# Kernel tuning notes

Hardware: AMD Instinct MI355X
Metric: run time of the kernel (lower is better)

Reference implementation:

```python
import jax, jax.numpy as jnp
import numpy as np

TOP_K = 4  # config.ffn_config.moe_top_k


def setup_inputs() -> dict:
    key = jax.random.key(0)
    k1, k2, k3, k4 = jax.random.split(key, 4)
    T, D, I, E = 4096, 1024, 2048, 16
    hidden_states = jax.random.normal(k1, (T, D), dtype=jnp.float32)
    router_w = jax.random.normal(k2, (E, D), dtype=jnp.float32) * 0.02
    # ws stacks [w1; v1] along output dim: [E, 2*I, D]
    ws = jax.random.normal(k3, (E, 2 * I, D), dtype=jnp.float32) * 0.02
    # w2s: [E, D, I]
    w2s = jax.random.normal(k4, (E, D, I), dtype=jnp.float32) * 0.02
    return {"hidden_states": hidden_states, "router_w": router_w, "ws": ws, "w2s": w2s}


def reference(hidden_states, router_w, ws, w2s):
    T, D = hidden_states.shape
    E = router_w.shape[0]
    I = ws.shape[1] // 2

    # Router: ReplicatedLinear(d_model -> num_experts), no bias
    router_logits = hidden_states @ router_w.T                      # [T, E]

    # fused_moe gating: softmax over all experts, top-k, renormalize
    probs = jax.nn.softmax(router_logits, axis=-1)                  # [T, E]
    topk_vals, topk_idx = jax.lax.top_k(probs, TOP_K)               # [T, K]
    topk_vals = topk_vals / jnp.sum(topk_vals, axis=-1, keepdims=True)
    # dense gate matrix [T, E]: selected experts get renormalized weight, else 0
    gates = jnp.zeros((T, E), dtype=hidden_states.dtype)
    gates = gates.at[jnp.arange(T)[:, None], topk_idx].set(topk_vals)

    h = jnp.einsum('td,eid->tei', hidden_states, ws)                # [T, E, 2I]
    act = jax.nn.silu(h[..., :I]) * h[..., I:]                      # [T, E, I]
    y = jnp.einsum('tei,edi->ted', act, w2s)                        # [T, E, D]

    # Combine: weighted sum over selected experts
    return jnp.einsum('ted,te->td', y, gates)                       # [T, D]
```

## Files before the change

kernel.cpp:

```cpp
#include <hip/hip_runtime.h>
#include <hip/hip_bf16.h>

#define T_TOK 4096
#define D_MODEL 1024
#define I_DIM 2048
#define E_EXP 16

typedef __bf16 bf16x8 __attribute__((ext_vector_type(8)));
typedef float f32x4 __attribute__((ext_vector_type(4)));

__device__ __forceinline__ bf16x8 pack8(f32x4 a, f32x4 b) {
    bf16x8 r;
    r[0] = (__bf16)a[0]; r[1] = (__bf16)a[1]; r[2] = (__bf16)a[2]; r[3] = (__bf16)a[3];
    r[4] = (__bf16)b[0]; r[5] = (__bf16)b[1]; r[6] = (__bf16)b[2]; r[7] = (__bf16)b[3];
    return r;
}

__device__ __forceinline__ void gl2lds(const __bf16* src, __bf16* dst) {
    __builtin_amdgcn_global_load_lds(
        (const __attribute__((address_space(1))) unsigned int*)src,
        (__attribute__((address_space(3))) unsigned int*)dst, 16, 0, 0);
}

__global__ __launch_bounds__(256) void cvt_kernel(
    const float* __restrict__ in, __bf16* __restrict__ out, int n8)
{
    const int stride = gridDim.x * 256;
    for (int i = blockIdx.x * 256 + threadIdx.x; i < n8; i += stride) {
        f32x4 a = ((const f32x4*)in)[i * 2];
        f32x4 b = ((const f32x4*)in)[i * 2 + 1];
        ((bf16x8*)out)[i] = pack8(a, b);
    }
}

__global__ __launch_bounds__(256) void router_fused_kernel(
    const float* __restrict__ x, const float* __restrict__ rw,
    unsigned int* __restrict__ choices, float* __restrict__ gate4,
    __bf16* __restrict__ x_bf, const float* __restrict__ wsw, __bf16* __restrict__ ws_bf)
{
    const int b = blockIdx.x;
    if (b >= 1280) {
        const int n8 = E_EXP * 2 * I_DIM * D_MODEL / 8;
        for (int i = (b - 1280) * 256 + threadIdx.x; i < n8; i += 2048 * 256) {
            f32x4 a = ((const f32x4*)wsw)[i * 2];
            f32x4 c = ((const f32x4*)wsw)[i * 2 + 1];
            ((bf16x8*)ws_bf)[i] = pack8(a, c);
        }
        return;
    }
    if (b >= 1024) {
        const int n8 = T_TOK * D_MODEL / 8;
        for (int i = (b - 1024) * 256 + threadIdx.x; i < n8; i += 256 * 256) {
            f32x4 a = ((const f32x4*)x)[i * 2];
            f32x4 c = ((const f32x4*)x)[i * 2 + 1];
            ((bf16x8*)x_bf)[i] = pack8(a, c);
        }
        return;
    }
    const int wid = threadIdx.x >> 6, lane = threadIdx.x & 63;
    const int t = b * 4 + wid;
    const int e = lane & 15, part = lane >> 4;

    const float* xr = x + (size_t)t * D_MODEL + part * 256;
    const float* wr = rw + (size_t)e * D_MODEL + part * 256;
    double acc = 0.0;
    #pragma unroll 4
    for (int i = 0; i < 256; i += 4) {
        f32x4 xv = *(const f32x4*)(xr + i);
        f32x4 wv = *(const f32x4*)(wr + i);
        acc += (double)xv[0] * wv[0] + (double)xv[1] * wv[1]
             + (double)xv[2] * wv[2] + (double)xv[3] * wv[3];
    }
    acc += __shfl_xor(acc, 16, 64);
    acc += __shfl_xor(acc, 32, 64);

    __shared__ float logits[4][16];
    if (lane < 16) logits[wid][lane] = (float)acc;
    __syncthreads();

    if (lane == 0) {
        float l[16];
        #pragma unroll
        for (int i = 0; i < 16; i++) l[i] = logits[wid][i];
        int idx[4]; float val[4];
        unsigned taken = 0;
        for (int k = 0; k < 4; k++) {
            int best = 0; float bv = -1e30f;
            for (int i = 0; i < 16; i++)
                if (!((taken >> i) & 1) && l[i] > bv) { bv = l[i]; best = i; }
            idx[k] = best; val[k] = bv; taken |= (1u << best);
        }
        const float m = val[0];
        float w[4], s = 0.f;
        for (int k = 0; k < 4; k++) { w[k] = __expf(val[k] - m); s += w[k]; }
        choices[t] = (unsigned)idx[0] | ((unsigned)idx[1] << 4)
                   | ((unsigned)idx[2] << 8) | ((unsigned)idx[3] << 12);
        f32x4 g = {w[0] / s, w[1] / s, w[2] / s, w[3] / s};
        *(f32x4*)(gate4 + t * 4) = g;
    }
}

__global__ __launch_bounds__(256) void build_lists_kernel(
    const unsigned int* __restrict__ choices, const float* __restrict__ gate4,
    int* __restrict__ counts, int* __restrict__ tok_list, float* __restrict__ gate_list)
{
    const int e = blockIdx.x;
    const int tid = threadIdx.x, lane = tid & 63, w = tid >> 6;
    __shared__ int wave_cnt[4];
    __shared__ int running;
    if (tid == 0) running = 0;
    __syncthreads();
    for (int chunk = 0; chunk < T_TOK; chunk += 256) {
        const int t = chunk + tid;
        const unsigned int ch = choices[t];
        int k = -1;
        #pragma unroll
        for (int kk = 0; kk < 4; ++kk)
            if (((ch >> (4 * kk)) & 15u) == (unsigned)e) k = kk;
        const unsigned long long m = __ballot(k >= 0);
        const int my = __popcll(m & ((1ull << lane) - 1ull));
        if (lane == 0) wave_cnt[w] = __popcll(m);
        __syncthreads();
        int base = running;
        #pragma unroll
        for (int i = 0; i < 4; ++i) if (i < w) base += wave_cnt[i];
        if (k >= 0) {
            const int slot = base + my;
            tok_list[e * T_TOK + slot] = t;
            gate_list[e * T_TOK + slot] = gate4[t * 4 + k];
        }
        __syncthreads();
        if (tid == 0) running += wave_cnt[0] + wave_cnt[1] + wave_cnt[2] + wave_cnt[3];
        __syncthreads();
    }
    if (tid == 0) counts[e] = running;
}

__global__ void prefix_kernel(const int* __restrict__ counts, int* __restrict__ prefix) {
    if (threadIdx.x == 0) {
        int acc = 0;
        for (int e = 0; e < E_EXP; e++) { prefix[e] = acc; acc += (counts[e] + 255) & ~255; }
        prefix[E_EXP] = acc;
    }
}

__global__ __launch_bounds__(256, 3) void gemm1_kernel(
    const __bf16* __restrict__ xb, const __bf16* __restrict__ wsb,
    const int* __restrict__ counts, const int* __restrict__ prefix,
    const int* __restrict__ tok_list, __bf16* __restrict__ act)
{
    const int q8 = gridDim.x >> 3;
    const int lid = (blockIdx.x & 7) * q8 + (blockIdx.x >> 3);
    const int e = lid >> 9;
    const int r = lid & 511;
    const int tileM = r & 15;
    const int tileN = r >> 4;

    const int count = counts[e];
    if (tileM * 128 >= count) return;

    const int tid = threadIdx.x;
    const int lane = tid & 63, w = tid >> 6;
    const int l15 = lane & 15, q = lane >> 4, l7 = lane & 7;
    const int wm = w >> 1, wc = w & 1;

    __shared__ __bf16 As[128 * 64];
    __shared__ __bf16 Bs[128 * 64];

    const int rl = lane >> 3;
    const int lc = (lane & 7) ^ rl;
    const __bf16* ptrA[4]; const __bf16* ptrB[4];
    #pragma unroll
    for (int i = 0; i < 4; ++i) {
        int grow = tileM * 128 + w * 32 + i * 8 + rl;
        if (grow >= count) grow = count - 1;
        const int token = tok_list[e * T_TOK + grow];
        ptrA[i] = xb + (size_t)token * D_MODEL + lc * 8;
        const int sub = w * 32 + i * 8 + rl;
        const int gcol = (sub < 64) ? (tileN * 64 + sub) : (I_DIM + tileN * 64 + (sub - 64));
        ptrB[i] = wsb + ((size_t)e * 2 * I_DIM + gcol) * D_MODEL + lc * 8;
    }
    __bf16* dA = &As[w * 2048];
    __bf16* dB = &Bs[w * 2048];

    #define STAGE(koff) do { \
        _Pragma("unroll") \
        for (int i_ = 0; i_ < 4; ++i_) gl2lds(ptrA[i_] + (koff), dA + i_ * 512); \
        _Pragma("unroll") \
        for (int i_ = 0; i_ < 4; ++i_) gl2lds(ptrB[i_] + (koff), dB + i_ * 512); \
    } while (0)

    f32x4 acc[4][4];
    const f32x4 z = {0.f, 0.f, 0.f, 0.f};
    #pragma unroll
    for (int mi = 0; mi < 4; ++mi)
        #pragma unroll
        for (int nj = 0; nj < 4; ++nj) acc[mi][nj] = z;

    const int c0 = (q ^ l7) * 8, c1 = ((4 + q) ^ l7) * 8;
    const int aoff = (wm * 64 + l15) * 64;
    const int boff = (wc * 32 + l15) * 64;

    STAGE(0);
    for (int kt = 0; kt < 16; ++kt) {
        __syncthreads();
        bf16x8 a0[4], a1[4], b0[4], b1[4];
        #pragma unroll
        for (int mi = 0; mi < 4; ++mi) {
            a0[mi] = *(const bf16x8*)&As[aoff + mi * 1024 + c0];
            a1[mi] = *(const bf16x8*)&As[aoff + mi * 1024 + c1];
        }
        #pragma unroll
        for (int nj = 0; nj < 2; ++nj) {
            b0[nj]     = *(const bf16x8*)&Bs[boff + nj * 1024 + c0];
            b0[nj + 2] = *(const bf16x8*)&Bs[boff + 4096 + nj * 1024 + c0];
            b1[nj]     = *(const bf16x8*)&Bs[boff + nj * 1024 + c1];
            b1[nj + 2] = *(const bf16x8*)&Bs[boff + 4096 + nj * 1024 + c1];
        }
        __syncthreads();
        if (kt + 1 < 16) STAGE((kt + 1) * 64);
        #pragma unroll
        for (int mi = 0; mi < 4; ++mi)
            #pragma unroll
            for (int nj = 0; nj < 4; ++nj) {
                acc[mi][nj] = __builtin_amdgcn_mfma_f32_16x16x32_bf16(a0[mi], b0[nj], acc[mi][nj], 0, 0, 0);
                acc[mi][nj] = __builtin_amdgcn_mfma_f32_16x16x32_bf16(a1[mi], b1[nj], acc[mi][nj], 0, 0, 0);
            }
    }
    #undef STAGE

    const int abase = prefix[e];
    #pragma unroll
    for (int mi = 0; mi < 4; ++mi) {
        #pragma unroll
        for (int j = 0; j < 4; ++j) {
            const int grow = tileM * 128 + wm * 64 + mi * 16 + q * 4 + j;
            if (grow < count) {
                __bf16* arowp = act + (size_t)(abase + grow) * I_DIM + tileN * 64 + wc * 32 + l15;
                #pragma unroll
                for (int nj = 0; nj < 2; ++nj) {
                    const float v1 = acc[mi][nj][j];
                    const float v2 = acc[mi][nj + 2][j];
                    arowp[nj * 16] = (__bf16)(v1 / (1.f + __expf(-v1)) * v2);
                }
            }
        }
    }
}

__global__ __launch_bounds__(256, 3) void gemm2_kernel(
    const __bf16* __restrict__ act, const __bf16* __restrict__ w2b,
    const int* __restrict__ counts, const int* __restrict__ prefix,
    const int* __restrict__ tok_list, const float* __restrict__ gate_list,
    float* __restrict__ out)
{
    const int q8 = gridDim.x >> 3;
    const int lid = (blockIdx.x & 7) * q8 + (blockIdx.x >> 3);
    const int e = lid >> 8;
    const int r = lid & 255;
    const int tileM = r & 15;
    const int tileN = (r >> 4) & 7;
    const int h = r >> 7;

    const int count = counts[e];
    if (tileM * 128 >= count) return;

    const int tid = threadIdx.x;
    const int lane = tid & 63, w = tid >> 6;
    const int l15 = lane & 15, q = lane >> 4, l7 = lane & 7;
    const int wm = w >> 1, wc = w & 1;
    const int abase = prefix[e];

    __shared__ __bf16 As[128 * 64];
    __shared__ __bf16 Bs[128 * 64];

    const int rl = lane >> 3;
    const int lc = (lane & 7) ^ rl;
    const __bf16* ptrA[4]; const __bf16* ptrB[4];
    #pragma unroll
    for (int i = 0; i < 4; ++i) {
        const int ar = tileM * 128 + w * 32 + i * 8 + rl;
        ptrA[i] = act + (size_t)(abase + ar) * I_DIM + h * 1024 + lc * 8;
        const int dcol = tileN * 128 + w * 32 + i * 8 + rl;
        ptrB[i] = w2b + ((size_t)e * D_MODEL + dcol) * I_DIM + h * 1024 + lc * 8;
    }
    __bf16* dA = &As[w * 2048];
    __bf16* dB = &Bs[w * 2048];

    #define STAGE(koff) do { \
        _Pragma("unroll") \
        for (int i_ = 0; i_ < 4; ++i_) gl2lds(ptrA[i_] + (koff), dA + i_ * 512); \
        _Pragma("unroll") \
        for (int i_ = 0; i_ < 4; ++i_) gl2lds(ptrB[i_] + (koff), dB + i_ * 512); \
    } while (0)

    f32x4 acc[4][4];
    const f32x4 z = {0.f, 0.f, 0.f, 0.f};
    #pragma unroll
    for (int mi = 0; mi < 4; ++mi)
        #pragma unroll
        for (int nj = 0; nj < 4; ++nj) acc[mi][nj] = z;

    const int c0 = (q ^ l7) * 8, c1 = ((4 + q) ^ l7) * 8;
    const int aoff = (wm * 64 + l15) * 64;
    const int boff = (wc * 64 + l15) * 64;

    STAGE(0);
    for (int kt = 0; kt < 16; ++kt) {
        __syncthreads();
        bf16x8 a0[4], a1[4], b0[4], b1[4];
        #pragma unroll
        for (int mi = 0; mi < 4; ++mi) {
            a0[mi] = *(const bf16x8*)&As[aoff + mi * 1024 + c0];
            a1[mi] = *(const bf16x8*)&As[aoff + mi * 1024 + c1];
        }
        #pragma unroll
        for (int nj = 0; nj < 4; ++nj) {
            b0[nj] = *(const bf16x8*)&Bs[boff + nj * 1024 + c0];
            b1[nj] = *(const bf16x8*)&Bs[boff + nj * 1024 + c1];
        }
        __syncthreads();
        if (kt + 1 < 16) STAGE((kt + 1) * 64);
        #pragma unroll
        for (int mi = 0; mi < 4; ++mi)
            #pragma unroll
            for (int nj = 0; nj < 4; ++nj) {
                acc[mi][nj] = __builtin_amdgcn_mfma_f32_16x16x32_bf16(a0[mi], b0[nj], acc[mi][nj], 0, 0, 0);
                acc[mi][nj] = __builtin_amdgcn_mfma_f32_16x16x32_bf16(a1[mi], b1[nj], acc[mi][nj], 0, 0, 0);
            }
    }
    #undef STAGE

    #pragma unroll
    for (int mi = 0; mi < 4; ++mi) {
        #pragma unroll
        for (int j = 0; j < 4; ++j) {
            const int grow = tileM * 128 + wm * 64 + mi * 16 + q * 4 + j;
            if (grow < count) {
                const int token = tok_list[e * T_TOK + grow];
                const float gate = gate_list[e * T_TOK + grow];
                float* orow = out + (size_t)token * D_MODEL + tileN * 128 + wc * 64 + l15;
                #pragma unroll
                for (int nj = 0; nj < 4; ++nj)
                    atomicAdd(orow + nj * 16, gate * acc[mi][nj][j]);
            }
        }
    }
}

extern "C" void kernel_launch(void* const* d_in, const int* in_sizes, int n_in,
                              void* d_out, int out_size, void* d_ws, size_t ws_size,
                              hipStream_t stream)
{
    const float* x   = (const float*)d_in[0];
    const float* rw  = (const float*)d_in[1];
    const float* wsw = (const float*)d_in[2];
    const float* w2s = (const float*)d_in[3];
    float* out = (float*)d_out;

    char* wsb = (char*)d_ws;
    int* counts        = (int*)wsb;
    int* prefix        = (int*)(wsb + 128);
    int* tok_list      = (int*)(wsb + 1024);
    float* gate_list   = (float*)(wsb + 1024 + E_EXP * T_TOK * 4);
    unsigned* choices  = (unsigned*)(wsb + 544u * 1024);
    float* gate4       = (float*)(wsb + 576u * 1024);
    __bf16* x_bf       = (__bf16*)(wsb + (1u << 20));
    __bf16* act        = (__bf16*)(wsb + (12u << 20));
    __bf16* ws_bf      = (__bf16*)(wsb + (96u << 20));
    __bf16* w2_bf      = ws_bf;

    hipMemsetAsync(d_out, 0, (size_t)out_size * sizeof(float), stream);

    router_fused_kernel<<<dim3(3328), 256, 0, stream>>>(x, rw, choices, gate4, x_bf, wsw, ws_bf);
    build_lists_kernel<<<dim3(E_EXP), 256, 0, stream>>>(choices, gate4, counts, tok_list, gate_list);
    prefix_kernel<<<1, 64, 0, stream>>>(counts, prefix);

    gemm1_kernel<<<dim3(8192), 256, 0, stream>>>(
        x_bf, ws_bf, counts, prefix, tok_list, act);

    cvt_kernel<<<8192, 256, 0, stream>>>(w2s, w2_bf, E_EXP * D_MODEL * I_DIM / 8);

    gemm2_kernel<<<dim3(4096), 256, 0, stream>>>(
        act, w2_bf, counts, prefix, tok_list, gate_list, out);
}
```

Before: 502.8 us.

## Replace atomic scatter in gemm2 with per-slot partial outputs and a combine pass

The second GEMM no longer splits K into two halves, and it stops atomically adding gated results into the output. Each token/top-k slot now writes its gated expert output to a dedicated row of a partial buffer, indexed by a new k-index list built alongside the token lists. A new combine kernel sums the four partial rows per token into the output, and the output memset is removed. This trades float atomics and the K-split for an extra 64 MB write plus read pass and half as many gemm2 blocks.

```diff
diff --git a/kernel.cpp b/kernel.cpp
--- a/kernel.cpp
+++ b/kernel.cpp
@@ -102,7 +102,8 @@
 
 __global__ __launch_bounds__(256) void build_lists_kernel(
     const unsigned int* __restrict__ choices, const float* __restrict__ gate4,
-    int* __restrict__ counts, int* __restrict__ tok_list, float* __restrict__ gate_list)
+    int* __restrict__ counts, int* __restrict__ tok_list, float* __restrict__ gate_list,
+    int* __restrict__ kidx_list)
 {
     const int e = blockIdx.x;
     const int tid = threadIdx.x, lane = tid & 63, w = tid >> 6;
@@ -128,6 +129,7 @@
             const int slot = base + my;
             tok_list[e * T_TOK + slot] = t;
             gate_list[e * T_TOK + slot] = gate4[t * 4 + k];
+            kidx_list[e * T_TOK + slot] = k;
         }
         __syncthreads();
         if (tid == 0) running += wave_cnt[0] + wave_cnt[1] + wave_cnt[2] + wave_cnt[3];
@@ -252,15 +254,14 @@
     const __bf16* __restrict__ act, const __bf16* __restrict__ w2b,
     const int* __restrict__ counts, const int* __restrict__ prefix,
     const int* __restrict__ tok_list, const float* __restrict__ gate_list,
-    float* __restrict__ out)
+    const int* __restrict__ kidx_list, float* __restrict__ ypart)
 {
     const int q8 = gridDim.x >> 3;
     const int lid = (blockIdx.x & 7) * q8 + (blockIdx.x >> 3);
-    const int e = lid >> 8;
-    const int r = lid & 255;
+    const int e = lid >> 7;
+    const int r = lid & 127;
     const int tileM = r & 15;
-    const int tileN = (r >> 4) & 7;
-    const int h = r >> 7;
+    const int tileN = r >> 4;
 
     const int count = counts[e];
     if (tileM * 128 >= count) return;
@@ -280,9 +281,9 @@
     #pragma unroll
     for (int i = 0; i < 4; ++i) {
         const int ar = tileM * 128 + w * 32 + i * 8 + rl;
-        ptrA[i] = act + (size_t)(abase + ar) * I_DIM + h * 1024 + lc * 8;
+        ptrA[i] = act + (size_t)(abase + ar) * I_DIM + lc * 8;
         const int dcol = tileN * 128 + w * 32 + i * 8 + rl;
-        ptrB[i] = w2b + ((size_t)e * D_MODEL + dcol) * I_DIM + h * 1024 + lc * 8;
+        ptrB[i] = w2b + ((size_t)e * D_MODEL + dcol) * I_DIM + lc * 8;
     }
     __bf16* dA = &As[w * 2048];
     __bf16* dB = &Bs[w * 2048];
@@ -306,7 +307,7 @@
     const int boff = (wc * 64 + l15) * 64;
 
     STAGE(0);
-    for (int kt = 0; kt < 16; ++kt) {
+    for (int kt = 0; kt < 32; ++kt) {
         __syncthreads();
         bf16x8 a0[4], a1[4], b0[4], b1[4];
         #pragma unroll
@@ -320,7 +321,7 @@
             b1[nj] = *(const bf16x8*)&Bs[boff + nj * 1024 + c1];
         }
         __syncthreads();
-        if (kt + 1 < 16) STAGE((kt + 1) * 64);
+        if (kt + 1 < 32) STAGE((kt + 1) * 64);
         #pragma unroll
         for (int mi = 0; mi < 4; ++mi)
             #pragma unroll
@@ -338,14 +339,28 @@
             const int grow = tileM * 128 + wm * 64 + mi * 16 + q * 4 + j;
             if (grow < count) {
                 const int token = tok_list[e * T_TOK + grow];
+                const int kk = kidx_list[e * T_TOK + grow];
                 const float gate = gate_list[e * T_TOK + grow];
-                float* orow = out + (size_t)token * D_MODEL + tileN * 128 + wc * 64 + l15;
+                float* orow = ypart + ((size_t)token * 4 + kk) * D_MODEL + tileN * 128 + wc * 64 + l15;
                 #pragma unroll
                 for (int nj = 0; nj < 4; ++nj)
-                    atomicAdd(orow + nj * 16, gate * acc[mi][nj][j]);
+                    orow[nj * 16] = gate * acc[mi][nj][j];
             }
         }
     }
+}
+
+__global__ __launch_bounds__(256) void combine_kernel(
+    const float* __restrict__ ypart, float* __restrict__ out)
+{
+    const int t = blockIdx.x;
+    const int d = threadIdx.x * 4;
+    const float* p = ypart + (size_t)t * 4 * D_MODEL;
+    f32x4 s = *(const f32x4*)(p + d);
+    s += *(const f32x4*)(p + D_MODEL + d);
+    s += *(const f32x4*)(p + 2 * D_MODEL + d);
+    s += *(const f32x4*)(p + 3 * D_MODEL + d);
+    *(f32x4*)(out + (size_t)t * D_MODEL + d) = s;
 }
 
 extern "C" void kernel_launch(void* const* d_in, const int* in_sizes, int n_in,
@@ -365,15 +380,15 @@
     float* gate_list   = (float*)(wsb + 1024 + E_EXP * T_TOK * 4);
     unsigned* choices  = (unsigned*)(wsb + 544u * 1024);
     float* gate4       = (float*)(wsb + 576u * 1024);
+    int* kidx_list     = (int*)(wsb + 640u * 1024);
     __bf16* x_bf       = (__bf16*)(wsb + (1u << 20));
     __bf16* act        = (__bf16*)(wsb + (12u << 20));
     __bf16* ws_bf      = (__bf16*)(wsb + (96u << 20));
     __bf16* w2_bf      = ws_bf;
-
-    hipMemsetAsync(d_out, 0, (size_t)out_size * sizeof(float), stream);
+    float* ypart       = (float*)(wsb + (160u << 20));
 
     router_fused_kernel<<<dim3(3328), 256, 0, stream>>>(x, rw, choices, gate4, x_bf, wsw, ws_bf);
-    build_lists_kernel<<<dim3(E_EXP), 256, 0, stream>>>(choices, gate4, counts, tok_list, gate_list);
+    build_lists_kernel<<<dim3(E_EXP), 256, 0, stream>>>(choices, gate4, counts, tok_list, gate_list, kidx_list);
     prefix_kernel<<<1, 64, 0, stream>>>(counts, prefix);
 
     gemm1_kernel<<<dim3(8192), 256, 0, stream>>>(
@@ -381,6 +396,8 @@
 
     cvt_kernel<<<8192, 256, 0, stream>>>(w2s, w2_bf, E_EXP * D_MODEL * I_DIM / 8);
 
-    gemm2_kernel<<<dim3(4096), 256, 0, stream>>>(
-        act, w2_bf, counts, prefix, tok_list, gate_list, out);
-}
+    gemm2_kernel<<<dim3(2048), 256, 0, stream>>>(
+        act, w2_bf, counts, prefix, tok_list, gate_list, kidx_list, ypart);
+
+    combine_kernel<<<dim3(T_TOK), 256, 0, stream>>>(ypart, out);
+}
```

New measurement: 444.0 us. 11.7% less time.
